# Optimization experiments

Measured on AMD Instinct MI355X. Metric: run time of the kernel, lower is better.

Reference implementation:

```python
import jax, jax.numpy as jnp
import numpy as np

N_EMBD = 1024
N_HEAD = 16
HEAD_DIM = N_EMBD // N_HEAD
B, T = 2, 2048
EPS = 1e-5


def _layernorm(x, gamma, beta):
    mu = jnp.mean(x, axis=-1, keepdims=True)
    var = jnp.mean((x - mu) ** 2, axis=-1, keepdims=True)
    return gamma * (x - mu) / jnp.sqrt(var + EPS) + beta


def setup_inputs() -> dict:
    key = jax.random.key(0)
    ks = jax.random.split(key, 12)
    s = 0.02
    d, f = N_EMBD, 4 * N_EMBD
    return {
        "x": jax.random.normal(ks[0], (B, T, d), dtype=jnp.float32),
        "ln1_g": jnp.ones((d,), jnp.float32),
        "ln1_b": jnp.zeros((d,), jnp.float32),
        "wq": jax.random.normal(ks[1], (d, d), jnp.float32) * s,
        "bq": jnp.zeros((d,), jnp.float32),
        "wk": jax.random.normal(ks[2], (d, d), jnp.float32) * s,
        "bk": jnp.zeros((d,), jnp.float32),
        "wv": jax.random.normal(ks[3], (d, d), jnp.float32) * s,
        "bv": jnp.zeros((d,), jnp.float32),
        "wo": jax.random.normal(ks[4], (d, d), jnp.float32) * s,
        "bo": jnp.zeros((d,), jnp.float32),
        "ln2_g": jnp.ones((d,), jnp.float32),
        "ln2_b": jnp.zeros((d,), jnp.float32),
        "w1": jax.random.normal(ks[5], (d, f), jnp.float32) * s,
        "b1": jnp.zeros((f,), jnp.float32),
        "w2": jax.random.normal(ks[6], (f, d), jnp.float32) * s,
        "b2": jnp.zeros((d,), jnp.float32),
    }


def reference(x, ln1_g, ln1_b, wq, bq, wk, bk, wv, bv, wo, bo,
              ln2_g, ln2_b, w1, b1, w2, b2):
    Bn, Tn, C = x.shape
    # --- attention branch (dropout = identity, eval mode) ---
    xn = _layernorm(x, ln1_g, ln1_b)
    q = (xn @ wq + bq).reshape(Bn, Tn, N_HEAD, HEAD_DIM)
    k = (xn @ wk + bk).reshape(Bn, Tn, N_HEAD, HEAD_DIM)
    v = (xn @ wv + bv).reshape(Bn, Tn, N_HEAD, HEAD_DIM)
    scale = 1.0 / jnp.sqrt(jnp.float32(HEAD_DIM))
    scores = jnp.einsum("bqhd,bkhd->bhqk", q, k) * scale  # [B,H,T,T]
    causal = jnp.tril(jnp.ones((Tn, Tn), dtype=bool))
    scores = jnp.where(causal[None, None], scores, -jnp.inf)
    weights = jax.nn.softmax(scores, axis=-1)
    attn = jnp.einsum("bhqk,bkhd->bqhd", weights, v).reshape(Bn, Tn, C)
    x = x + (attn @ wo + bo)
    # --- MLP branch ---
    h = _layernorm(x, ln2_g, ln2_b)
    h = jax.nn.gelu(h @ w1 + b1, approximate=False)
    x = x + (h @ w2 + b2)
    return x
```

## Files before the change

### kernel.cpp

```cpp
#include <hip/hip_runtime.h>
#include <stdint.h>

#define T_SEQ 2048
#define NHEAD 16
#define HDIM 64
#define CDIM 1024
#define FDIM 4096
#define MROWS 4096
#define NQB 32

typedef __bf16 bf16;
typedef __bf16 bf16x8 __attribute__((ext_vector_type(8)));
typedef float f32x4 __attribute__((ext_vector_type(4)));

__device__ __forceinline__ void gload_lds16(const void* g, void* l) {
  __builtin_amdgcn_global_load_lds(
      (const __attribute__((address_space(1))) void*)g,
      (__attribute__((address_space(3))) void*)l, 16, 0, 0);
}

__device__ __forceinline__ void wt_body(const float* __restrict__ src,
                                        bf16* __restrict__ dst, int K, int N,
                                        int k0, int n0) {
  __shared__ float tile[64][65];
  int tid = threadIdx.x;
  int r4 = tid >> 4, c4 = (tid & 15) * 4;
#pragma unroll
  for (int p = 0; p < 4; ++p) {
    int r = p * 16 + r4;
    float4 v = *(const float4*)&src[(size_t)(k0 + r) * N + n0 + c4];
    tile[r][c4] = v.x; tile[r][c4 + 1] = v.y;
    tile[r][c4 + 2] = v.z; tile[r][c4 + 3] = v.w;
  }
  __syncthreads();
  int n8 = tid >> 3, k8 = (tid & 7) * 8;
#pragma unroll
  for (int p = 0; p < 2; ++p) {
    int n = p * 32 + n8;
    union { bf16 h[8]; uint4 u; } t;
#pragma unroll
    for (int j = 0; j < 8; ++j) t.h[j] = (bf16)tile[k8 + j][n];
    *(uint4*)&dst[(size_t)(n0 + n) * K + k0 + k8] = t.u;
  }
}

__global__ void wt_kernel(const float* __restrict__ src, bf16* __restrict__ dst,
                          int K, int N) {
  wt_body(src, dst, K, N, blockIdx.y * 64, blockIdx.x * 64);
}

__global__ void wt4_kernel(const float* s0, const float* s1, const float* s2,
                           const float* s3, bf16* d0, bf16* d1, bf16* d2, bf16* d3) {
  const float* src = blockIdx.z == 0 ? s0 : blockIdx.z == 1 ? s1 : blockIdx.z == 2 ? s2 : s3;
  bf16* dst = blockIdx.z == 0 ? d0 : blockIdx.z == 1 ? d1 : blockIdx.z == 2 ? d2 : d3;
  wt_body(src, dst, 1024, 1024, blockIdx.y * 64, blockIdx.x * 64);
}

__global__ void vt_kernel(const bf16* __restrict__ v, bf16* __restrict__ vt) {
  __shared__ bf16 tile[64][65];
  int bh = blockIdx.y;
  int t0 = blockIdx.x * 64;
  int tid = threadIdx.x;
  const bf16* src = v + (size_t)bh * T_SEQ * HDIM;
  bf16* dst = vt + (size_t)bh * HDIM * T_SEQ;
  int r8 = tid >> 3, c8 = (tid & 7) * 8;
#pragma unroll
  for (int p = 0; p < 2; ++p) {
    int r = p * 32 + r8;
    union { uint4 u; bf16 h[8]; } t;
    t.u = *(const uint4*)&src[(size_t)(t0 + r) * HDIM + c8];
#pragma unroll
    for (int j = 0; j < 8; ++j) tile[r][c8 + j] = t.h[j];
  }
  __syncthreads();
#pragma unroll
  for (int p = 0; p < 2; ++p) {
    int d = p * 32 + r8;
    union { uint4 u; bf16 h[8]; } t;
#pragma unroll
    for (int j = 0; j < 8; ++j) t.h[j] = tile[c8 + j][d];
    *(uint4*)&dst[(size_t)d * T_SEQ + t0 + c8] = t.u;
  }
}

__global__ __launch_bounds__(256)
void ln_kernel(const float* __restrict__ x, const float* __restrict__ g,
               const float* __restrict__ b, bf16* __restrict__ out) {
  int row = blockIdx.x;
  int tid = threadIdx.x;
  float4 v = *(const float4*)&x[(size_t)row * CDIM + tid * 4];
  float s = v.x + v.y + v.z + v.w;
  float ss = v.x * v.x + v.y * v.y + v.z * v.z + v.w * v.w;
#pragma unroll
  for (int off = 1; off < 64; off <<= 1) {
    s += __shfl_xor(s, off, 64);
    ss += __shfl_xor(ss, off, 64);
  }
  __shared__ float red[8];
  int wv = tid >> 6, ln = tid & 63;
  if (ln == 0) { red[wv] = s; red[4 + wv] = ss; }
  __syncthreads();
  s = red[0] + red[1] + red[2] + red[3];
  ss = red[4] + red[5] + red[6] + red[7];
  float mu = s * (1.0f / CDIM);
  float var = ss * (1.0f / CDIM) - mu * mu;
  float rstd = rsqrtf(var + 1e-5f);
  float4 gv = *(const float4*)&g[tid * 4];
  float4 bv = *(const float4*)&b[tid * 4];
  union { bf16 h[4]; uint2 u; } o;
  o.h[0] = (bf16)(gv.x * (v.x - mu) * rstd + bv.x);
  o.h[1] = (bf16)(gv.y * (v.y - mu) * rstd + bv.y);
  o.h[2] = (bf16)(gv.z * (v.z - mu) * rstd + bv.z);
  o.h[3] = (bf16)(gv.w * (v.w - mu) * rstd + bv.w);
  *(uint2*)&out[(size_t)row * CDIM + tid * 4] = o.u;
}

__global__ __launch_bounds__(256)
void addp_kernel(float* __restrict__ out, const float* __restrict__ p1, int n4) {
  int i = blockIdx.x * 256 + threadIdx.x;
  int stride = gridDim.x * 256;
  for (; i < n4; i += stride) {
    f32x4 a = *(const f32x4*)&out[i * 4];
    f32x4 b = *(const f32x4*)&p1[i * 4];
    a += b;
    *(f32x4*)&out[i * 4] = a;
  }
}

enum { EPI_QKV = 0, EPI_F32RES = 1, EPI_GELU = 2, EPI_SPLIT = 3 };

template <int EPI, int BN>
__global__ __launch_bounds__(512, 1)
void gemm256(const bf16* __restrict__ A, const bf16* __restrict__ Bt,
             const float* __restrict__ bias, const float* __restrict__ bias2,
             const float* __restrict__ bias3, const float* res,
             void* outp, void* out2, void* out3, int M, int N, int K, int Kstride) {
  constexpr int WCOLS = BN / 64;
  constexpr int WROWS = 8 / WCOLS;
  constexpr int MR = (256 / WROWS) / 16;
  constexpr int MH = MR / 2;
  constexpr int BCH = BN / 128;
  __shared__ __align__(16) bf16 As[3][256 * 32];
  __shared__ __align__(16) bf16 Bs[3][BN * 32];
  int tid = threadIdx.x;
  int w = tid >> 6, l = tid & 63;
  int wr = w / WCOLS, wc = w % WCOLS;
  int lo = l & 15, g = l >> 4;

  int nwg = gridDim.x * gridDim.y;
  int orig = blockIdx.y * gridDim.x + blockIdx.x;
  int lid = (orig & 7) * (nwg >> 3) + (orig >> 3);
  int bx = lid % gridDim.x, by = lid / gridDim.x;
  int m0 = by * 256, n0 = bx * BN;
  int koff = blockIdx.z * K;

  f32x4 acc[MR][4];
#pragma unroll
  for (int i = 0; i < MR; ++i)
#pragma unroll
    for (int j = 0; j < 4; ++j) acc[i][j] = (f32x4){0.f, 0.f, 0.f, 0.f};

  const bf16* Ab = A + (size_t)m0 * Kstride + koff;
  const bf16* Bb = Bt + (size_t)n0 * Kstride + koff;

  int srow = tid >> 2;
  int scol = ((tid & 3) ^ ((tid >> 3) & 3)) * 8;
  auto STAGE_A = [&](int t, int buf) {
    int k0 = t * 32;
#pragma unroll
    for (int c = 0; c < 2; ++c)
      gload_lds16(Ab + (size_t)(c * 128 + srow) * Kstride + k0 + scol,
                  &As[buf][c * 4096 + w * 512]);
  };
  auto STAGE_B = [&](int t, int buf) {
    int k0 = t * 32;
#pragma unroll
    for (int c = 0; c < BCH; ++c)
      gload_lds16(Bb + (size_t)(c * 128 + srow) * Kstride + k0 + scol,
                  &Bs[buf][c * 4096 + w * 512]);
  };

  int nt = K >> 5;
  STAGE_A(0, 0); STAGE_B(0, 0);
  STAGE_A(1, 1); STAGE_B(1, 1);
  if constexpr (BN == 256) asm volatile("s_waitcnt vmcnt(4)" ::: "memory");
  else                     asm volatile("s_waitcnt vmcnt(3)" ::: "memory");
  __syncthreads();
  int sw = (lo >> 1) & 3;
  int b0 = 0;
  for (int t = 0; t < nt; ++t) {
    int b2 = b0 - 1; if (b2 < 0) b2 += 3;
    bf16x8 af[MH], bfr[4];
#pragma unroll
    for (int m = 0; m < MH; ++m) {
      int R = wr * (MR * 16) + m * 16 + lo;
      af[m] = *(const bf16x8*)&As[b0][R * 32 + (g ^ sw) * 8];
    }
#pragma unroll
    for (int n = 0; n < 4; ++n) {
      int R = wc * 64 + n * 16 + lo;
      bfr[n] = *(const bf16x8*)&Bs[b0][R * 32 + (g ^ sw) * 8];
    }
    if (t + 2 < nt) STAGE_A(t + 2, b2);
    asm volatile("s_barrier" ::: "memory");
    __builtin_amdgcn_s_setprio(1);
#pragma unroll
    for (int m = 0; m < MH; ++m)
#pragma unroll
      for (int n = 0; n < 4; ++n)
        acc[m][n] = __builtin_amdgcn_mfma_f32_16x16x32_bf16(af[m], bfr[n], acc[m][n], 0, 0, 0);
    __builtin_amdgcn_s_setprio(0);
#pragma unroll
    for (int m = 0; m < MH; ++m) {
      int R = wr * (MR * 16) + (m + MH) * 16 + lo;
      af[m] = *(const bf16x8*)&As[b0][R * 32 + (g ^ sw) * 8];
    }
    if (t + 2 < nt) {
      STAGE_B(t + 2, b2);
      if constexpr (BN == 256) asm volatile("s_waitcnt vmcnt(4)" ::: "memory");
      else                     asm volatile("s_waitcnt vmcnt(3)" ::: "memory");
    } else if (t + 1 < nt) {
      asm volatile("s_waitcnt vmcnt(0)" ::: "memory");
    }
    asm volatile("s_barrier" ::: "memory");
    __builtin_amdgcn_s_setprio(1);
#pragma unroll
    for (int m = 0; m < MH; ++m)
#pragma unroll
      for (int n = 0; n < 4; ++n)
        acc[m + MH][n] = __builtin_amdgcn_mfma_f32_16x16x32_bf16(af[m], bfr[n], acc[m + MH][n], 0, 0, 0);
    __builtin_amdgcn_s_setprio(0);
    b0 = (b0 == 2) ? 0 : b0 + 1;
  }

  if constexpr (EPI == EPI_QKV) {
    int which = n0 >> 10;
    const float* bb = which == 0 ? bias : (which == 1 ? bias2 : bias3);
    bf16* ob = (bf16*)(which == 0 ? outp : (which == 1 ? out2 : out3));
#pragma unroll
    for (int m = 0; m < MR; ++m)
#pragma unroll
      for (int n = 0; n < 4; ++n)
#pragma unroll
        for (int j = 0; j < 4; ++j) {
          int row = m0 + wr * (MR * 16) + m * 16 + g * 4 + j;
          int col = n0 + wc * 64 + n * 16 + lo;
          int cw = col & (CDIM - 1);
          float v = acc[m][n][j] + bb[cw];
          int b = row >> 11, tt = row & (T_SEQ - 1);
          int h = cw >> 6, d = cw & (HDIM - 1);
          ob[(((size_t)(b * NHEAD + h)) * T_SEQ + tt) * HDIM + d] = (bf16)v;
        }
  } else if constexpr (EPI == EPI_SPLIT) {
#pragma unroll
    for (int m = 0; m < MR; ++m)
#pragma unroll
      for (int n = 0; n < 4; ++n)
#pragma unroll
        for (int j = 0; j < 4; ++j) {
          int row = m0 + wr * (MR * 16) + m * 16 + g * 4 + j;
          int col = n0 + wc * 64 + n * 16 + lo;
          if (blockIdx.z == 0) {
            float v = acc[m][n][j] + bias[col];
            ((float*)outp)[(size_t)row * N + col] = v + res[(size_t)row * N + col];
          } else {
            ((float*)out2)[(size_t)row * N + col] = acc[m][n][j];
          }
        }
  } else {
#pragma unroll
    for (int m = 0; m < MR; ++m)
#pragma unroll
      for (int n = 0; n < 4; ++n)
#pragma unroll
        for (int j = 0; j < 4; ++j) {
          int row = m0 + wr * (MR * 16) + m * 16 + g * 4 + j;
          int col = n0 + wc * 64 + n * 16 + lo;
          float v = acc[m][n][j] + bias[col];
          if constexpr (EPI == EPI_F32RES) {
            ((float*)outp)[(size_t)row * N + col] = v + res[(size_t)row * N + col];
          } else {
            float ge = 0.5f * v * (1.0f + erff(v * 0.70710678118654752f));
            ((bf16*)outp)[(size_t)row * N + col] = (bf16)ge;
          }
        }
  }
}

template <int EPI, int TN>
__global__ __launch_bounds__(256, 2)
void gemm_bt(const bf16* __restrict__ A, const bf16* __restrict__ Bt,
             const float* __restrict__ bias, const float* __restrict__ bias2,
             const float* __restrict__ bias3, const float* res,
             void* outp, void* out2, void* out3, int M, int N, int K, int Kstride) {
  constexpr int MR = (TN == 128) ? 4 : 2;
  __shared__ __align__(16) bf16 As[4][128 * 32];
  __shared__ __align__(16) bf16 Bs[4][TN * 32];
  int tid = threadIdx.x;
  int w = tid >> 6, l = tid & 63;
  int lo = l & 15, g = l >> 4;
  int rowb = (TN == 128) ? (w >> 1) * 64 : w * 32;
  int colb = (TN == 128) ? (w & 1) * 64 : 0;

  int nwg = gridDim.x * gridDim.y;
  int orig = blockIdx.y * gridDim.x + blockIdx.x;
  int lid = (orig & 7) * (nwg >> 3) + (orig >> 3);
  int bx = lid % gridDim.x, by = lid / gridDim.x;
  int m0 = by * 128, n0 = bx * TN;

  f32x4 acc[MR][4];
#pragma unroll
  for (int i = 0; i < MR; ++i)
#pragma unroll
    for (int j = 0; j < 4; ++j) acc[i][j] = (f32x4){0.f, 0.f, 0.f, 0.f};

  const bf16* Ab = A + (size_t)m0 * Kstride;
  const bf16* Bb = Bt + (size_t)n0 * Kstride;

  auto STAGE = [&](int t, int buf) {
    int k0 = t * 32;
    int row = (l >> 2);
    int col = ((l & 3) ^ ((l >> 3) & 3)) * 8;
#pragma unroll
    for (int i = 0; i < 2; ++i) {
      int c = w * 2 + i;
      gload_lds16(Ab + (size_t)(c * 16 + row) * Kstride + k0 + col, &As[buf][c * 512]);
    }
    if constexpr (TN == 128) {
#pragma unroll
      for (int i = 0; i < 2; ++i) {
        int c = w * 2 + i;
        gload_lds16(Bb + (size_t)(c * 16 + row) * Kstride + k0 + col, &Bs[buf][c * 512]);
      }
    } else {
      int c = w;
      gload_lds16(Bb + (size_t)(c * 16 + row) * Kstride + k0 + col, &Bs[buf][c * 512]);
    }
  };

  int nt = K >> 5;
  STAGE(0, 0);
  STAGE(1, 1);
  STAGE(2, 2);
  int sw = (lo >> 1) & 3;
  for (int t = 0; t < nt; ++t) {
    if constexpr (TN == 128) {
      if (t + 2 < nt)      asm volatile("s_waitcnt vmcnt(8)" ::: "memory");
      else if (t + 1 < nt) asm volatile("s_waitcnt vmcnt(4)" ::: "memory");
      else                 asm volatile("s_waitcnt vmcnt(0)" ::: "memory");
    } else {
      if (t + 2 < nt)      asm volatile("s_waitcnt vmcnt(6)" ::: "memory");
      else if (t + 1 < nt) asm volatile("s_waitcnt vmcnt(3)" ::: "memory");
      else                 asm volatile("s_waitcnt vmcnt(0)" ::: "memory");
    }
    __builtin_amdgcn_s_barrier();
    __builtin_amdgcn_sched_barrier(0);
    int cur = t & 3;
    bf16x8 af[MR], bfr[4];
#pragma unroll
    for (int m = 0; m < MR; ++m) {
      int R = rowb + m * 16 + lo;
      af[m] = *(const bf16x8*)&As[cur][R * 32 + (g ^ sw) * 8];
    }
#pragma unroll
    for (int n = 0; n < 4; ++n) {
      int R = colb + n * 16 + lo;
      bfr[n] = *(const bf16x8*)&Bs[cur][R * 32 + (g ^ sw) * 8];
    }
    if (t + 3 < nt) STAGE(t + 3, (t + 3) & 3);
    __builtin_amdgcn_s_setprio(1);
#pragma unroll
    for (int m = 0; m < MR; ++m)
#pragma unroll
      for (int n = 0; n < 4; ++n)
        acc[m][n] = __builtin_amdgcn_mfma_f32_16x16x32_bf16(af[m], bfr[n], acc[m][n], 0, 0, 0);
    __builtin_amdgcn_s_setprio(0);
  }

#pragma unroll
  for (int m = 0; m < MR; ++m)
#pragma unroll
    for (int n = 0; n < 4; ++n)
#pragma unroll
      for (int j = 0; j < 4; ++j) {
        int row = m0 + rowb + m * 16 + g * 4 + j;
        int col = n0 + colb + n * 16 + lo;
        float v = acc[m][n][j] + bias[col];
        if constexpr (EPI == EPI_F32RES) {
          ((float*)outp)[(size_t)row * N + col] = v + res[(size_t)row * N + col];
        } else {
          float ge = 0.5f * v * (1.0f + erff(v * 0.70710678118654752f));
          ((bf16*)outp)[(size_t)row * N + col] = (bf16)ge;
        }
      }
}

__device__ __forceinline__ void attn_tile(
    const bf16* __restrict__ Ksb, const bf16* __restrict__ Vsb,
    bf16* __restrict__ Psw, const bf16x8 qf[2], f32x4 Ot[4],
    float& mrun, float& lrun, int lo, int g, int kbase, int myq, bool diag) {
  f32x4 st[4];
#pragma unroll
  for (int kt = 0; kt < 4; ++kt) {
    f32x4 a = (f32x4){0.f, 0.f, 0.f, 0.f};
#pragma unroll
    for (int dh = 0; dh < 2; ++dh) {
      int R = kt * 16 + lo;
      int slot = (dh * 4 + g) ^ (R & 7);
      bf16x8 kf = *(const bf16x8*)&Ksb[R * 64 + slot * 8];
      a = __builtin_amdgcn_mfma_f32_16x16x32_bf16(kf, qf[dh], a, 0, 0, 0);
    }
    st[kt] = a;
  }
  if (diag) {
#pragma unroll
    for (int kt = 0; kt < 4; ++kt)
#pragma unroll
      for (int j = 0; j < 4; ++j) {
        int key = kbase + kt * 16 + g * 4 + j;
        if (key > myq) st[kt][j] = -1e30f;
      }
  }
  float cmax = -1e30f;
#pragma unroll
  for (int kt = 0; kt < 4; ++kt)
#pragma unroll
    for (int j = 0; j < 4; ++j) cmax = fmaxf(cmax, st[kt][j]);
  cmax = fmaxf(cmax, __shfl_xor(cmax, 16, 64));
  cmax = fmaxf(cmax, __shfl_xor(cmax, 32, 64));
  float mnew = fmaxf(mrun, cmax);
  float corr = exp2f(mrun - mnew);
  float csum = 0.f;
#pragma unroll
  for (int kt = 0; kt < 4; ++kt) {
    union { bf16 h[4]; uint2 u; } pk;
#pragma unroll
    for (int j = 0; j < 4; ++j) {
      float pv = exp2f(st[kt][j] - mnew);
      csum += pv;
      pk.h[j] = (bf16)pv;
    }
    *(uint2*)&Psw[lo * 72 + kt * 16 + g * 4] = pk.u;
  }
  csum += __shfl_xor(csum, 16, 64);
  csum += __shfl_xor(csum, 32, 64);
  lrun = lrun * corr + csum;
  mrun = mnew;
#pragma unroll
  for (int dt = 0; dt < 4; ++dt)
#pragma unroll
    for (int j = 0; j < 4; ++j) Ot[dt][j] *= corr;
#pragma unroll
  for (int ks = 0; ks < 2; ++ks) {
    bf16x8 pf = *(const bf16x8*)&Psw[lo * 72 + ks * 32 + g * 8];
#pragma unroll
    for (int dt = 0; dt < 4; ++dt) {
      int R = dt * 16 + lo;
      int slot = (ks * 4 + g) ^ (R & 7);
      bf16x8 vf = *(const bf16x8*)&Vsb[R * 64 + slot * 8];
      Ot[dt] = __builtin_amdgcn_mfma_f32_16x16x32_bf16(vf, pf, Ot[dt], 0, 0, 0);
    }
  }
}

__global__ __launch_bounds__(256, 2)
void attn_kernel(const bf16* __restrict__ q, const bf16* __restrict__ k,
                 const bf16* __restrict__ vt, bf16* __restrict__ out) {
  __shared__ __align__(16) bf16 Ks[2][64 * 64];
  __shared__ __align__(16) bf16 Vs[2][64 * 64];
  __shared__ __align__(16) bf16 Ps[4][16 * 72];
  int tid = threadIdx.x;
  int w = tid >> 6, l = tid & 63;
  int lo = l & 15, g = l >> 4;
  int nwg = gridDim.x * gridDim.y;
  int orig = blockIdx.y * gridDim.x + blockIdx.x;
  int lid = (orig & 7) * (nwg >> 3) + (orig >> 3);
  int p = lid & 15;
  int bh = lid >> 4;
  int qA = p, qB = NQB - 1 - p;
  int nch = qB + 1;
  const bf16* qh = q + (size_t)bh * T_SEQ * HDIM;
  const bf16* kh = k + (size_t)bh * T_SEQ * HDIM;
  const bf16* vh = vt + (size_t)bh * HDIM * T_SEQ;

  const float sc = 0.125f * 1.44269504f;
  bf16x8 qfA[2], qfB[2];
#pragma unroll
  for (int dh = 0; dh < 2; ++dh) {
    bf16x8 tA = *(const bf16x8*)&qh[(size_t)(qA * 64 + w * 16 + lo) * HDIM + dh * 32 + g * 8];
    bf16x8 tB = *(const bf16x8*)&qh[(size_t)(qB * 64 + w * 16 + lo) * HDIM + dh * 32 + g * 8];
#pragma unroll
    for (int j = 0; j < 8; ++j) {
      qfA[dh][j] = (bf16)((float)tA[j] * sc);
      qfB[dh][j] = (bf16)((float)tB[j] * sc);
    }
  }
  int myqA = qA * 64 + w * 16 + lo;
  int myqB = qB * 64 + w * 16 + lo;

  f32x4 OtA[4], OtB[4];
#pragma unroll
  for (int i = 0; i < 4; ++i) {
    OtA[i] = (f32x4){0.f, 0.f, 0.f, 0.f};
    OtB[i] = (f32x4){0.f, 0.f, 0.f, 0.f};
  }
  float mA = -1e30f, lA = 0.f, mB = -1e30f, lB = 0.f;

  int srow8 = l >> 3, s0 = l & 7;
  auto STAGE = [&](int kc, int buf) {
#pragma unroll
    for (int i = 0; i < 2; ++i) {
      int c = w * 2 + i;
      int r = c * 8 + srow8;
      int ecol = (s0 ^ (r & 7)) * 8;
      gload_lds16(&kh[(size_t)(kc * 64 + r) * HDIM + ecol], &Ks[buf][c * 512]);
      gload_lds16(&vh[(size_t)r * T_SEQ + kc * 64 + ecol], &Vs[buf][c * 512]);
    }
  };

  STAGE(0, 0);
  int cur = 0;
  for (int kc = 0; kc < nch; ++kc) {
    __syncthreads();
    if (kc + 1 < nch) STAGE(kc + 1, cur ^ 1);
    attn_tile(Ks[cur], Vs[cur], Ps[w], qfB, OtB, mB, lB, lo, g, kc * 64, myqB,
              kc == nch - 1);
    if (kc <= p)
      attn_tile(Ks[cur], Vs[cur], Ps[w], qfA, OtA, mA, lA, lo, g, kc * 64, myqA,
                kc == p);
    cur ^= 1;
  }

  int b = bh >> 4, h = bh & 15;
  {
    float inv = 1.0f / lA;
    bf16* ob = out + (((size_t)b * T_SEQ + myqA) * NHEAD + h) * HDIM;
#pragma unroll
    for (int dt = 0; dt < 4; ++dt)
#pragma unroll
      for (int j = 0; j < 4; ++j) ob[dt * 16 + g * 4 + j] = (bf16)(OtA[dt][j] * inv);
  }
  {
    float inv = 1.0f / lB;
    bf16* ob = out + (((size_t)b * T_SEQ + myqB) * NHEAD + h) * HDIM;
#pragma unroll
    for (int dt = 0; dt < 4; ++dt)
#pragma unroll
      for (int j = 0; j < 4; ++j) ob[dt * 16 + g * 4 + j] = (bf16)(OtB[dt][j] * inv);
  }
}

extern "C" void kernel_launch(void* const* d_in, const int* in_sizes, int n_in,
                              void* d_out, int out_size, void* d_ws, size_t ws_size,
                              hipStream_t stream) {
  (void)in_sizes; (void)n_in; (void)out_size; (void)ws_size;
  const float* x     = (const float*)d_in[0];
  const float* ln1_g = (const float*)d_in[1];
  const float* ln1_b = (const float*)d_in[2];
  const float* wq    = (const float*)d_in[3];
  const float* bq    = (const float*)d_in[4];
  const float* wk    = (const float*)d_in[5];
  const float* bk    = (const float*)d_in[6];
  const float* wv    = (const float*)d_in[7];
  const float* bv    = (const float*)d_in[8];
  const float* wo    = (const float*)d_in[9];
  const float* bo    = (const float*)d_in[10];
  const float* ln2_g = (const float*)d_in[11];
  const float* ln2_b = (const float*)d_in[12];
  const float* w1    = (const float*)d_in[13];
  const float* b1    = (const float*)d_in[14];
  const float* w2    = (const float*)d_in[15];
  const float* b2    = (const float*)d_in[16];
  float* out = (float*)d_out;

  const size_t MB = 1024ull * 1024ull;
  char* ws = (char*)d_ws;
  bf16* wqkvT = (bf16*)(ws + 0 * MB);
  bf16* wqT = wqkvT;
  bf16* wkT = (bf16*)(ws + 2 * MB);
  bf16* wvT = (bf16*)(ws + 4 * MB);
  bf16* woT = (bf16*)(ws + 6 * MB);
  bf16* w1T = (bf16*)(ws + 8 * MB);
  bf16* w2T = (bf16*)(ws + 16 * MB);
  bf16* xn  = (bf16*)(ws + 24 * MB);
  bf16* qb_ = (bf16*)(ws + 32 * MB);
  bf16* kb_ = (bf16*)(ws + 40 * MB);
  bf16* vb_ = (bf16*)(ws + 48 * MB);
  bf16* vtb = (bf16*)(ws + 56 * MB);
  bf16* aout = (bf16*)(ws + 24 * MB);
  bf16* hn  = (bf16*)(ws + 32 * MB);
  bf16* hb  = (bf16*)(ws + 40 * MB);
  float* p1 = (float*)(ws + 24 * MB);

  dim3 blk(256);
  wt4_kernel<<<dim3(16, 16, 4), blk, 0, stream>>>(wq, wk, wv, wo, wqT, wkT, wvT, woT);
  wt_kernel<<<dim3(64, 16), blk, 0, stream>>>(w1, w1T, 1024, 4096);
  wt_kernel<<<dim3(16, 64), blk, 0, stream>>>(w2, w2T, 4096, 1024);

  ln_kernel<<<MROWS, blk, 0, stream>>>(x, ln1_g, ln1_b, xn);

  gemm256<EPI_QKV, 256><<<dim3(12, 16), dim3(512), 0, stream>>>(
      xn, wqkvT, bq, bk, bv, nullptr, qb_, kb_, vb_, MROWS, 3 * CDIM, CDIM, CDIM);

  vt_kernel<<<dim3(32, 32), blk, 0, stream>>>(vb_, vtb);
  attn_kernel<<<dim3(16, 32), blk, 0, stream>>>(qb_, kb_, vtb, aout);

  gemm_bt<EPI_F32RES, 64><<<dim3(16, 32), blk, 0, stream>>>(
      aout, woT, bo, nullptr, nullptr, x, out, nullptr, nullptr, MROWS, CDIM, CDIM, CDIM);

  ln_kernel<<<MROWS, blk, 0, stream>>>(out, ln2_g, ln2_b, hn);

  gemm256<EPI_GELU, 256><<<dim3(16, 16), dim3(512), 0, stream>>>(
      hn, w1T, b1, nullptr, nullptr, nullptr, hb, nullptr, nullptr, MROWS, FDIM, CDIM, CDIM);

  gemm256<EPI_SPLIT, 128><<<dim3(8, 16, 2), dim3(512), 0, stream>>>(
      hb, w2T, b2, nullptr, nullptr, out, out, p1, nullptr, MROWS, CDIM, FDIM / 2, FDIM);
  addp_kernel<<<2048, blk, 0, stream>>>(out, p1, MROWS * CDIM / 4);
}
```

Before: 246.2 us.

## Add lazy softmax rescaling, tanh GELU and padded P-tile stride

The attention inner tile now skips the running-max update and the rescale of O and l unless some lane's new block max exceeds the current max by more than 8 (log2 units). This removes an exp2 and 16 multiplies per tile in the common case, at the cost of P values up to 2^8 stored in bf16. The exact erf GELU in the FC1 epilogue is replaced by an exp2-based tanh approximation, trading a small deviation from the exact-GELU reference for cheaper math. The P scratch row stride changes from 72 to 76 elements to alter the LDS bank mapping, but this leaves the 16-byte vector reads only 8-byte aligned.

```diff
diff --git a/kernel.cpp b/kernel.cpp
--- a/kernel.cpp
+++ b/kernel.cpp
@@ -8,6 +8,7 @@
 #define FDIM 4096
 #define MROWS 4096
 #define NQB 32
+#define PSTR 76
 
 typedef __bf16 bf16;
 typedef __bf16 bf16x8 __attribute__((ext_vector_type(8)));
@@ -17,6 +18,13 @@
   __builtin_amdgcn_global_load_lds(
       (const __attribute__((address_space(1))) void*)g,
       (__attribute__((address_space(3))) void*)l, 16, 0, 0);
+}
+
+__device__ __forceinline__ float gelu_tanh(float v) {
+  float u = 0.7978845608f * (v + 0.044715f * v * v * v);
+  float e = exp2f(u * 2.885390082f);
+  float th = 1.0f - 2.0f / (e + 1.0f);
+  return 0.5f * v * (1.0f + th);
 }
 
 __device__ __forceinline__ void wt_body(const float* __restrict__ src,
@@ -280,8 +288,7 @@
           if constexpr (EPI == EPI_F32RES) {
             ((float*)outp)[(size_t)row * N + col] = v + res[(size_t)row * N + col];
           } else {
-            float ge = 0.5f * v * (1.0f + erff(v * 0.70710678118654752f));
-            ((bf16*)outp)[(size_t)row * N + col] = (bf16)ge;
+            ((bf16*)outp)[(size_t)row * N + col] = (bf16)gelu_tanh(v);
           }
         }
   }
@@ -389,8 +396,7 @@
         if constexpr (EPI == EPI_F32RES) {
           ((float*)outp)[(size_t)row * N + col] = v + res[(size_t)row * N + col];
         } else {
-          float ge = 0.5f * v * (1.0f + erff(v * 0.70710678118654752f));
-          ((bf16*)outp)[(size_t)row * N + col] = (bf16)ge;
+          ((bf16*)outp)[(size_t)row * N + col] = (bf16)gelu_tanh(v);
         }
       }
 }
@@ -421,38 +427,41 @@
         if (key > myq) st[kt][j] = -1e30f;
       }
   }
-  float cmax = -1e30f;
-#pragma unroll
-  for (int kt = 0; kt < 4; ++kt)
-#pragma unroll
-    for (int j = 0; j < 4; ++j) cmax = fmaxf(cmax, st[kt][j]);
+  float cmax = fmaxf(fmaxf(fmaxf(st[0][0], st[0][1]), fmaxf(st[0][2], st[0][3])),
+                     fmaxf(fmaxf(st[1][0], st[1][1]), fmaxf(st[1][2], st[1][3])));
+  float cmax2 = fmaxf(fmaxf(fmaxf(st[2][0], st[2][1]), fmaxf(st[2][2], st[2][3])),
+                      fmaxf(fmaxf(st[3][0], st[3][1]), fmaxf(st[3][2], st[3][3])));
+  cmax = fmaxf(cmax, cmax2);
   cmax = fmaxf(cmax, __shfl_xor(cmax, 16, 64));
   cmax = fmaxf(cmax, __shfl_xor(cmax, 32, 64));
-  float mnew = fmaxf(mrun, cmax);
-  float corr = exp2f(mrun - mnew);
+  if (!__all(cmax <= mrun + 8.0f)) {
+    float mnew = fmaxf(mrun, cmax);
+    float corr = exp2f(mrun - mnew);
+    lrun *= corr;
+#pragma unroll
+    for (int dt = 0; dt < 4; ++dt)
+#pragma unroll
+      for (int j = 0; j < 4; ++j) Ot[dt][j] *= corr;
+    mrun = mnew;
+  }
   float csum = 0.f;
 #pragma unroll
   for (int kt = 0; kt < 4; ++kt) {
     union { bf16 h[4]; uint2 u; } pk;
 #pragma unroll
     for (int j = 0; j < 4; ++j) {
-      float pv = exp2f(st[kt][j] - mnew);
+      float pv = exp2f(st[kt][j] - mrun);
       csum += pv;
       pk.h[j] = (bf16)pv;
     }
-    *(uint2*)&Psw[lo * 72 + kt * 16 + g * 4] = pk.u;
+    *(uint2*)&Psw[lo * PSTR + kt * 16 + g * 4] = pk.u;
   }
   csum += __shfl_xor(csum, 16, 64);
   csum += __shfl_xor(csum, 32, 64);
-  lrun = lrun * corr + csum;
-  mrun = mnew;
-#pragma unroll
-  for (int dt = 0; dt < 4; ++dt)
-#pragma unroll
-    for (int j = 0; j < 4; ++j) Ot[dt][j] *= corr;
+  lrun += csum;
 #pragma unroll
   for (int ks = 0; ks < 2; ++ks) {
-    bf16x8 pf = *(const bf16x8*)&Psw[lo * 72 + ks * 32 + g * 8];
+    bf16x8 pf = *(const bf16x8*)&Psw[lo * PSTR + ks * 32 + g * 8];
 #pragma unroll
     for (int dt = 0; dt < 4; ++dt) {
       int R = dt * 16 + lo;
@@ -468,7 +477,7 @@
                  const bf16* __restrict__ vt, bf16* __restrict__ out) {
   __shared__ __align__(16) bf16 Ks[2][64 * 64];
   __shared__ __align__(16) bf16 Vs[2][64 * 64];
-  __shared__ __align__(16) bf16 Ps[4][16 * 72];
+  __shared__ __align__(16) bf16 Ps[4][16 * PSTR];
   int tid = threadIdx.x;
   int w = tid >> 6, l = tid & 63;
   int lo = l & 15, g = l >> 4;
```

Measured after the change: 249.3 us. No clear change (+1.3%).
